# Optimization experiments

Measured on AMD Instinct MI355X. Metric: run time of the kernel, lower is better.

The kernel has to match this reference:

```python
import jax, jax.numpy as jnp
import numpy as np

B, S, D = 1, 2048, 2048
H, KV, HD = 16, 4, 128
HALF = HD // 2
REP = H // KV
LAMBDA_INIT = 0.5
OUT_SCALE = 1.0 - LAMBDA_INIT


def _rope(x, cos, sin):
    # x: (B, S, heads, HD); cos/sin: (S, HD//2). Complex pair rotation on
    # interleaved (even, odd) channels, matching torch.view_as_complex.
    orig_shape = x.shape
    xp = x.reshape(*x.shape[:-1], -1, 2)
    x0, x1 = xp[..., 0], xp[..., 1]
    c = cos[None, :, None, :]
    s = sin[None, :, None, :]
    r0 = x0 * c - x1 * s
    r1 = x0 * s + x1 * c
    return jnp.stack([r0, r1], axis=-1).reshape(orig_shape)


def _sdpa_causal(q, k, v, scale):
    # q,k: (B, S, H, half), v: (B, S, H, HD). Causal softmax attention.
    scores = jnp.einsum('bshd,bthd->bhst', q, k) * scale
    causal = jnp.tril(jnp.ones((S, S), dtype=bool))
    scores = jnp.where(causal[None, None, :, :], scores, jnp.finfo(scores.dtype).min)
    p = jax.nn.softmax(scores, axis=-1)
    return jnp.einsum('bhst,bthd->bshd', p, v)


def setup_inputs() -> dict:
    key = jax.random.key(0)
    ks = jax.random.split(key, 7)
    x = jax.random.normal(ks[0], (B, S, D), dtype=jnp.float32)
    # RoPE frequencies: theta_i = 10000^(-2i/HD), angles = pos * theta
    inv_freq = 1.0 / (10000.0 ** (np.arange(0, HD, 2, dtype=np.float32) / HD))
    angles = np.arange(S, dtype=np.float32)[:, None] * inv_freq[None, :]
    freqs_cos = jnp.asarray(np.cos(angles), dtype=jnp.float32)
    freqs_sin = jnp.asarray(np.sin(angles), dtype=jnp.float32)
    sd = 0.02
    Wq = jax.random.normal(ks[1], (D, H * HD), dtype=jnp.float32) * sd
    Wk = jax.random.normal(ks[2], (D, KV * HD), dtype=jnp.float32) * sd
    Wv = jax.random.normal(ks[3], (D, KV * HD), dtype=jnp.float32) * sd
    Wo = jax.random.normal(ks[4], (H * HD, D), dtype=jnp.float32) * sd
    lam0 = float(np.log(LAMBDA_INIT / (1.0 - LAMBDA_INIT)))
    lambda_param = jnp.full((H,), lam0, dtype=jnp.float32)
    return {'x': x, 'freqs_cos': freqs_cos, 'freqs_sin': freqs_sin,
            'Wq': Wq, 'Wk': Wk, 'Wv': Wv, 'Wo': Wo, 'lambda_param': lambda_param}


def reference(x, freqs_cos, freqs_sin, Wq, Wk, Wv, Wo, lambda_param):
    q = (x @ Wq).reshape(B, S, H, HD)
    k = (x @ Wk).reshape(B, S, KV, HD)
    v = (x @ Wv).reshape(B, S, KV, HD)
    q = _rope(q, freqs_cos, freqs_sin)
    k = _rope(k, freqs_cos, freqs_sin)
    # GQA expansion: each kv head repeated REP times consecutively
    k = jnp.repeat(k, REP, axis=2)
    v = jnp.repeat(v, REP, axis=2)
    q1, q2 = q[..., :HALF], q[..., HALF:]
    k1, k2 = k[..., :HALF], k[..., HALF:]
    scale = 1.0 / jnp.sqrt(jnp.float32(HALF))  # SDPA scales by query last dim
    a1 = _sdpa_causal(q1, k1, v, scale)  # (B, S, H, HD)
    a2 = _sdpa_causal(q2, k2, v, scale)
    lam = jax.nn.sigmoid(lambda_param).astype(x.dtype)[None, None, :, None]
    out = (a1 - lam * a2) * OUT_SCALE
    out = out.reshape(B, S, H * HD)
    return out @ Wo
```

## Files before the change

### kernel.cpp

```cpp
#include <hip/hip_runtime.h>
#include <hip/hip_bf16.h>
#include <cstdint>

typedef __bf16 bf16_t;
typedef __attribute__((ext_vector_type(8))) __bf16 bf16x8;
typedef __attribute__((ext_vector_type(4))) __bf16 bf16x4;
typedef __attribute__((ext_vector_type(4))) float f32x4;

#define S_LEN 2048
#define D_MODEL 2048
#define NH 16
#define NKV 4
#define HD_ 128

#define MFMA16(a, b, c) __builtin_amdgcn_mfma_f32_16x16x32_bf16((a), (b), (c), 0, 0, 0)

__device__ __forceinline__ void gload_lds16(const void* g, void* l) {
  __builtin_amdgcn_global_load_lds((__attribute__((address_space(1))) void*)((void*)g),
                                   (__attribute__((address_space(3))) void*)(l), 16, 0, 0);
}

__global__ __launch_bounds__(256) void cast_x_kernel(const float* __restrict__ in,
                                                     bf16_t* __restrict__ out, int n8) {
  int i = blockIdx.x * 256 + threadIdx.x;
  if (i >= n8) return;
  float4 a = reinterpret_cast<const float4*>(in)[2 * i];
  float4 b = reinterpret_cast<const float4*>(in)[2 * i + 1];
  bf16x8 o = {(__bf16)a.x, (__bf16)a.y, (__bf16)a.z, (__bf16)a.w,
              (__bf16)b.x, (__bf16)b.y, (__bf16)b.z, (__bf16)b.w};
  *reinterpret_cast<bf16x8*>(out + (size_t)i * 8) = o;
}

__global__ __launch_bounds__(256) void transpose_cast64_kernel(const float* __restrict__ in,
    bf16_t* __restrict__ out, int ldin, int ldout) {
  __shared__ float t[64][65];
  const int c0 = blockIdx.x * 64, r0 = blockIdx.y * 64;
  const int rr = threadIdx.x >> 4;
  const int cc = (threadIdx.x & 15) * 4;
#pragma unroll
  for (int p = 0; p < 4; ++p) {
    int r = rr + p * 16;
    float4 v = *reinterpret_cast<const float4*>(in + (size_t)(r0 + r) * ldin + c0 + cc);
    t[r][cc] = v.x; t[r][cc + 1] = v.y; t[r][cc + 2] = v.z; t[r][cc + 3] = v.w;
  }
  __syncthreads();
  const int c = threadIdx.x >> 2;
  const int q = threadIdx.x & 3;
  bf16_t* orow = out + (size_t)(c0 + c) * ldout + r0 + q * 16;
#pragma unroll
  for (int half = 0; half < 2; ++half) {
    bf16x8 o;
#pragma unroll
    for (int j = 0; j < 8; ++j) o[j] = (__bf16)t[q * 16 + half * 8 + j][c];
    *reinterpret_cast<bf16x8*>(orow + half * 8) = o;
  }
}

#define SC_Q 0.18033688f

__global__ __launch_bounds__(256) void rope_kernel(const float* __restrict__ qkv,
    const float* __restrict__ cosT, const float* __restrict__ sinT,
    bf16_t* __restrict__ Qb, bf16_t* __restrict__ Kb) {
  const int s = blockIdx.x;
  const int tid = threadIdx.x;
  const int ch = tid & 15;
  float4 cs = *reinterpret_cast<const float4*>(cosT + s * 64 + ch * 4);
  float4 sn = *reinterpret_cast<const float4*>(sinT + s * 64 + ch * 4);
  {
    const int hq = tid >> 4;
    const float* src = qkv + (size_t)s * 3072 + hq * 128 + ch * 8;
    float4 a = *reinterpret_cast<const float4*>(src);
    float4 b = *reinterpret_cast<const float4*>(src + 4);
    bf16x8 o;
    o[0] = (__bf16)((a.x * cs.x - a.y * sn.x) * SC_Q);
    o[1] = (__bf16)((a.x * sn.x + a.y * cs.x) * SC_Q);
    o[2] = (__bf16)((a.z * cs.y - a.w * sn.y) * SC_Q);
    o[3] = (__bf16)((a.z * sn.y + a.w * cs.y) * SC_Q);
    o[4] = (__bf16)((b.x * cs.z - b.y * sn.z) * SC_Q);
    o[5] = (__bf16)((b.x * sn.z + b.y * cs.z) * SC_Q);
    o[6] = (__bf16)((b.z * cs.w - b.w * sn.w) * SC_Q);
    o[7] = (__bf16)((b.z * sn.w + b.w * cs.w) * SC_Q);
    *reinterpret_cast<bf16x8*>(Qb + ((size_t)hq * S_LEN + s) * HD_ + ch * 8) = o;
  }
  if (tid < 64) {
    const int kh = tid >> 4;
    const float* src = qkv + (size_t)s * 3072 + 2048 + kh * 128 + ch * 8;
    float4 a = *reinterpret_cast<const float4*>(src);
    float4 b = *reinterpret_cast<const float4*>(src + 4);
    bf16x8 o;
    o[0] = (__bf16)(a.x * cs.x - a.y * sn.x);
    o[1] = (__bf16)(a.x * sn.x + a.y * cs.x);
    o[2] = (__bf16)(a.z * cs.y - a.w * sn.y);
    o[3] = (__bf16)(a.z * sn.y + a.w * cs.y);
    o[4] = (__bf16)(b.x * cs.z - b.y * sn.z);
    o[5] = (__bf16)(b.x * sn.z + b.y * cs.z);
    o[6] = (__bf16)(b.z * cs.w - b.w * sn.w);
    o[7] = (__bf16)(b.z * sn.w + b.w * cs.w);
    *reinterpret_cast<bf16x8*>(Kb + ((size_t)kh * S_LEN + s) * HD_ + ch * 8) = o;
  }
}

#define BM 128
#define BK 64

template <int BNv>
__global__ __launch_bounds__(256) void gemm_bf16_kernel(const bf16_t* __restrict__ A,
    const bf16_t* __restrict__ B, float* __restrict__ C, int M, int N, int K) {
  constexpr int NF = BNv / 32;
  constexpr int BITER = BNv * 8 / 256;
  __shared__ __attribute__((aligned(16))) bf16_t aL[BM * BK];
  __shared__ __attribute__((aligned(16))) bf16_t bL[BNv * BK];
  const int tid = threadIdx.x;
  const int wave = tid >> 6, lane = tid & 63;
  const int wr = wave >> 1, wc = wave & 1;
  const int l15 = lane & 15, l4 = lane >> 4;
  const int bm = blockIdx.y * BM, bn = blockIdx.x * BNv;

  f32x4 zero = {0.f, 0.f, 0.f, 0.f};
  f32x4 acc[4][NF];
#pragma unroll
  for (int m = 0; m < 4; ++m)
#pragma unroll
    for (int n = 0; n < NF; ++n) acc[m][n] = zero;

  const bf16_t* aSrc[4];
  bf16_t* aDst[4];
#pragma unroll
  for (int i = 0; i < 4; ++i) {
    int ci = i * 256 + tid;
    int r = ci >> 3;
    int cl = (ci & 7) ^ (r & 7);
    aSrc[i] = A + (size_t)(bm + r) * K + cl * 8;
    aDst[i] = aL + (i * 256 + wave * 64) * 8;
  }
  const bf16_t* bSrc[BITER];
  bf16_t* bDst[BITER];
#pragma unroll
  for (int i = 0; i < BITER; ++i) {
    int ci = i * 256 + tid;
    int r = ci >> 3;
    int cl = (ci & 7) ^ (r & 7);
    bSrc[i] = B + (size_t)(bn + r) * K + cl * 8;
    bDst[i] = bL + (i * 256 + wave * 64) * 8;
  }

  for (int kt = 0; kt < K; kt += BK) {
#pragma unroll
    for (int i = 0; i < 4; ++i) gload_lds16(aSrc[i] + kt, aDst[i]);
#pragma unroll
    for (int i = 0; i < BITER; ++i) gload_lds16(bSrc[i] + kt, bDst[i]);
    __syncthreads();
#pragma unroll
    for (int t = 0; t < 2; ++t) {
      bf16x8 af[4], bfr[NF];
#pragma unroll
      for (int f = 0; f < 4; ++f) {
        int Ra = wr * 64 + f * 16 + l15;
        int ca = (t * 4 + l4) ^ (Ra & 7);
        af[f] = *reinterpret_cast<const bf16x8*>(aL + Ra * 64 + ca * 8);
      }
#pragma unroll
      for (int f = 0; f < NF; ++f) {
        int Rb = wc * (BNv / 2) + f * 16 + l15;
        int cb = (t * 4 + l4) ^ (Rb & 7);
        bfr[f] = *reinterpret_cast<const bf16x8*>(bL + Rb * 64 + cb * 8);
      }
      __builtin_amdgcn_s_setprio(1);
#pragma unroll
      for (int m = 0; m < 4; ++m)
#pragma unroll
        for (int n = 0; n < NF; ++n) acc[m][n] = MFMA16(af[m], bfr[n], acc[m][n]);
      __builtin_amdgcn_s_setprio(0);
    }
    __syncthreads();
  }

#pragma unroll
  for (int m = 0; m < 4; ++m) {
    int row0 = bm + wr * 64 + m * 16 + l4 * 4;
#pragma unroll
    for (int n = 0; n < NF; ++n) {
      int col = bn + wc * (BNv / 2) + n * 16 + l15;
#pragma unroll
      for (int r = 0; r < 4; ++r) C[(size_t)(row0 + r) * N + col] = acc[m][n][r];
    }
  }
}

__global__ __launch_bounds__(256) void diff_attn_kernel(const bf16_t* __restrict__ Qb,
    const bf16_t* __restrict__ Kb, const bf16_t* __restrict__ VTb,
    const float* __restrict__ lambda_param, bf16_t* __restrict__ attn) {
  const int b = blockIdx.x;
  const int p = b >> 1;
  const int h = p >> 4;
  const int tdx = p & 15;
  const int jt = (b & 1) ? tdx : (31 - tdx);
  const int kvh = h >> 2;
  const int tid = threadIdx.x, wave = tid >> 6, lane = tid & 63;
  const int l15 = lane & 15, l4 = lane >> 4;

  __shared__ __attribute__((aligned(16))) bf16_t kB[2][64 * 128];
  __shared__ __attribute__((aligned(16))) bf16_t vB[2][64 * 128];
  __shared__ __attribute__((aligned(16))) bf16_t pS[4][2][16 * 64];

  const bf16_t* kBase = Kb + (size_t)kvh * S_LEN * HD_;
  const bf16_t* vBase = VTb + (size_t)kvh * HD_ * S_LEN;
  int kOff[4], vOff[4], dOff[4];
#pragma unroll
  for (int i = 0; i < 4; ++i) {
    int ci = i * 256 + tid;
    int kr = ci >> 4;
    kOff[i] = kr * HD_ + (((ci & 15) ^ (kr & 7)) * 8);
    int vr = ci >> 3;
    vOff[i] = vr * S_LEN + (((ci & 7) ^ (vr & 7)) * 8);
    dOff[i] = (i * 256 + wave * 64) * 8;
  }

  const float lam = 1.f / (1.f + __expf(-lambda_param[h]));
  const f32x4 zero = {0.f, 0.f, 0.f, 0.f};

  const int q0 = jt * 64;
  const int qg = q0 + wave * 16 + l15;

  const bf16_t* qp = Qb + ((size_t)h * S_LEN + qg) * HD_;
  bf16x8 qf[4];
#pragma unroll
  for (int f = 0; f < 4; ++f) qf[f] = *reinterpret_cast<const bf16x8*>(qp + f * 32 + l4 * 8);

  f32x4 o1[8], o2[8];
#pragma unroll
  for (int n = 0; n < 8; ++n) { o1[n] = zero; o2[n] = zero; }
  float m1 = -__builtin_inff(), m2 = -__builtin_inff(), l1 = 0.f, l2 = 0.f;

#pragma unroll
  for (int i = 0; i < 4; ++i) gload_lds16(kBase + kOff[i], &kB[0][0] + dOff[i]);
#pragma unroll
  for (int i = 0; i < 4; ++i) gload_lds16(vBase + vOff[i], &vB[0][0] + dOff[i]);
  __syncthreads();

  for (int t = 0; t <= jt; ++t) {
    const int cur = t & 1;
    if (t < jt) {
      const size_t kv0n = (size_t)(t + 1) * 64;
#pragma unroll
      for (int i = 0; i < 4; ++i) gload_lds16(kBase + kv0n * HD_ + kOff[i], &kB[cur ^ 1][0] + dOff[i]);
#pragma unroll
      for (int i = 0; i < 4; ++i) gload_lds16(vBase + kv0n + vOff[i], &vB[cur ^ 1][0] + dOff[i]);
    }
    const bf16_t* kL = &kB[cur][0];
    const bf16_t* vL = &vB[cur][0];
    const int kv0 = t * 64;

    f32x4 s1[4], s2[4];
#pragma unroll
    for (int n = 0; n < 4; ++n) { s1[n] = zero; s2[n] = zero; }
    __builtin_amdgcn_s_setprio(1);
#pragma unroll
    for (int tt = 0; tt < 2; ++tt) {
#pragma unroll
      for (int n = 0; n < 4; ++n) {
        const int Rk = n * 16 + l15;
        bf16x8 kf1 = *reinterpret_cast<const bf16x8*>(kL + Rk * 128 + (((tt * 4 + l4) ^ (Rk & 7)) * 8));
        s1[n] = MFMA16(kf1, qf[tt], s1[n]);
      }
    }
#pragma unroll
    for (int tt = 0; tt < 2; ++tt) {
#pragma unroll
      for (int n = 0; n < 4; ++n) {
        const int Rk = n * 16 + l15;
        bf16x8 kf2 = *reinterpret_cast<const bf16x8*>(kL + Rk * 128 + (((8 + tt * 4 + l4) ^ (Rk & 7)) * 8));
        s2[n] = MFMA16(kf2, qf[2 + tt], s2[n]);
      }
    }
    __builtin_amdgcn_s_setprio(0);

    if (t == jt) {
#pragma unroll
      for (int n = 0; n < 4; ++n)
#pragma unroll
        for (int r = 0; r < 4; ++r)
          if (kv0 + n * 16 + l4 * 4 + r > qg) { s1[n][r] = -1e30f; s2[n][r] = -1e30f; }
    }

    {
      float ma[4];
#pragma unroll
      for (int n = 0; n < 4; ++n)
        ma[n] = fmaxf(fmaxf(s1[n][0], s1[n][1]), fmaxf(s1[n][2], s1[n][3]));
      float tmax = fmaxf(fmaxf(ma[0], ma[1]), fmaxf(ma[2], ma[3]));
      tmax = fmaxf(tmax, __shfl_xor(tmax, 16));
      tmax = fmaxf(tmax, __shfl_xor(tmax, 32));
      if (!__all(tmax <= m1 + 8.f)) {
        const float mn = fmaxf(m1, tmax);
        const float sc = __builtin_exp2f(m1 - mn);
        m1 = mn;
        l1 *= sc;
#pragma unroll
        for (int n = 0; n < 8; ++n) o1[n] *= sc;
      }
      float rsn[4];
#pragma unroll
      for (int n = 0; n < 4; ++n) {
        float e0 = __builtin_exp2f(s1[n][0] - m1);
        float e1 = __builtin_exp2f(s1[n][1] - m1);
        float e2 = __builtin_exp2f(s1[n][2] - m1);
        float e3 = __builtin_exp2f(s1[n][3] - m1);
        rsn[n] = (e0 + e1) + (e2 + e3);
        int cswz = (n * 2 + (l4 >> 1)) ^ (l15 & 7);
        bf16x4 pk = {(__bf16)e0, (__bf16)e1, (__bf16)e2, (__bf16)e3};
        *reinterpret_cast<bf16x4*>(&pS[wave][0][l15 * 64 + cswz * 8 + (l4 & 1) * 4]) = pk;
      }
      float rs = (rsn[0] + rsn[1]) + (rsn[2] + rsn[3]);
      rs += __shfl_xor(rs, 16);
      rs += __shfl_xor(rs, 32);
      l1 += rs;
    }
    {
      float ma[4];
#pragma unroll
      for (int n = 0; n < 4; ++n)
        ma[n] = fmaxf(fmaxf(s2[n][0], s2[n][1]), fmaxf(s2[n][2], s2[n][3]));
      float tmax = fmaxf(fmaxf(ma[0], ma[1]), fmaxf(ma[2], ma[3]));
      tmax = fmaxf(tmax, __shfl_xor(tmax, 16));
      tmax = fmaxf(tmax, __shfl_xor(tmax, 32));
      if (!__all(tmax <= m2 + 8.f)) {
        const float mn = fmaxf(m2, tmax);
        const float sc = __builtin_exp2f(m2 - mn);
        m2 = mn;
        l2 *= sc;
#pragma unroll
        for (int n = 0; n < 8; ++n) o2[n] *= sc;
      }
      float rsn[4];
#pragma unroll
      for (int n = 0; n < 4; ++n) {
        float e0 = __builtin_exp2f(s2[n][0] - m2);
        float e1 = __builtin_exp2f(s2[n][1] - m2);
        float e2 = __builtin_exp2f(s2[n][2] - m2);
        float e3 = __builtin_exp2f(s2[n][3] - m2);
        rsn[n] = (e0 + e1) + (e2 + e3);
        int cswz = (n * 2 + (l4 >> 1)) ^ (l15 & 7);
        bf16x4 pk = {(__bf16)e0, (__bf16)e1, (__bf16)e2, (__bf16)e3};
        *reinterpret_cast<bf16x4*>(&pS[wave][1][l15 * 64 + cswz * 8 + (l4 & 1) * 4]) = pk;
      }
      float rs = (rsn[0] + rsn[1]) + (rsn[2] + rsn[3]);
      rs += __shfl_xor(rs, 16);
      rs += __shfl_xor(rs, 32);
      l2 += rs;
    }

    __builtin_amdgcn_s_setprio(1);
#pragma unroll
    for (int kt = 0; kt < 2; ++kt) {
      int cp = ((kt * 4 + l4) ^ (l15 & 7)) * 8;
      bf16x8 pf1 = *reinterpret_cast<const bf16x8*>(&pS[wave][0][l15 * 64 + cp]);
      bf16x8 pf2 = *reinterpret_cast<const bf16x8*>(&pS[wave][1][l15 * 64 + cp]);
#pragma unroll
      for (int n = 0; n < 8; ++n) {
        const int Rv = n * 16 + l15;
        bf16x8 vf = *reinterpret_cast<const bf16x8*>(vL + Rv * 64 + (((kt * 4 + l4) ^ (Rv & 7)) * 8));
        o1[n] = MFMA16(vf, pf1, o1[n]);
        o2[n] = MFMA16(vf, pf2, o2[n]);
      }
    }
    __builtin_amdgcn_s_setprio(0);
    __syncthreads();
  }

  const float i1 = 1.f / l1, i2 = lam / l2;
  bf16_t* orow = attn + (size_t)qg * D_MODEL + h * HD_;
#pragma unroll
  for (int n = 0; n < 8; ++n) {
    bf16x4 w = {(__bf16)((o1[n][0] * i1 - o2[n][0] * i2) * 0.5f),
                (__bf16)((o1[n][1] * i1 - o2[n][1] * i2) * 0.5f),
                (__bf16)((o1[n][2] * i1 - o2[n][2] * i2) * 0.5f),
                (__bf16)((o1[n][3] * i1 - o2[n][3] * i2) * 0.5f)};
    *reinterpret_cast<bf16x4*>(orow + n * 16 + l4 * 4) = w;
  }
}

extern "C" void kernel_launch(void* const* d_in, const int* in_sizes, int n_in,
                              void* d_out, int out_size, void* d_ws, size_t ws_size,
                              hipStream_t stream) {
  const float* x    = (const float*)d_in[0];
  const float* fcos = (const float*)d_in[1];
  const float* fsin = (const float*)d_in[2];
  const float* Wq   = (const float*)d_in[3];
  const float* Wk   = (const float*)d_in[4];
  const float* Wv   = (const float*)d_in[5];
  const float* Wo   = (const float*)d_in[6];
  const float* lam  = (const float*)d_in[7];
  float* out = (float*)d_out;

  char* w = (char*)d_ws;
  bf16_t* xb    = (bf16_t*)(w);
  bf16_t* attnb = (bf16_t*)(w);
  bf16_t* WqkvT = (bf16_t*)(w + (8ull << 20));
  bf16_t* Qb    = (bf16_t*)(w + (8ull << 20));
  bf16_t* Kb    = (bf16_t*)(w + (16ull << 20));
  bf16_t* VT    = (bf16_t*)(w + (18ull << 20));
  bf16_t* WoT   = (bf16_t*)(w + (20ull << 20));
  float*  QKV   = (float*) (w + (28ull << 20));

  cast_x_kernel<<<2048, 256, 0, stream>>>(x, xb, 524288);
  transpose_cast64_kernel<<<dim3(32, 32), 256, 0, stream>>>(Wq, WqkvT, 2048, 2048);
  transpose_cast64_kernel<<<dim3(8, 32), 256, 0, stream>>>(Wk, WqkvT + 2048 * 2048, 512, 2048);
  transpose_cast64_kernel<<<dim3(8, 32), 256, 0, stream>>>(Wv, WqkvT + 2560 * 2048, 512, 2048);
  transpose_cast64_kernel<<<dim3(32, 32), 256, 0, stream>>>(Wo, WoT, 2048, 2048);

  gemm_bf16_kernel<64><<<dim3(48, 16), 256, 0, stream>>>(xb, WqkvT, QKV, 2048, 3072, 2048);

  rope_kernel<<<2048, 256, 0, stream>>>(QKV, fcos, fsin, Qb, Kb);
  transpose_cast64_kernel<<<dim3(8, 32), 256, 0, stream>>>(QKV + 2560, VT, 3072, 2048);

  diff_attn_kernel<<<512, 256, 0, stream>>>(Qb, Kb, VT, lam, attnb);

  gemm_bf16_kernel<64><<<dim3(32, 16), 256, 0, stream>>>(attnb, WoT, out, 2048, 2048, 2048);
}
```

Measured before the change: 286.5 us.

## Pair long and short causal query tiles per block and serialize the two softmax branches

After: 278.7 us. 1.03x faster.

```diff
diff --git a/kernel.cpp b/kernel.cpp
--- a/kernel.cpp
+++ b/kernel.cpp
@@ -190,18 +190,15 @@
 __global__ __launch_bounds__(256) void diff_attn_kernel(const bf16_t* __restrict__ Qb,
     const bf16_t* __restrict__ Kb, const bf16_t* __restrict__ VTb,
     const float* __restrict__ lambda_param, bf16_t* __restrict__ attn) {
-  const int b = blockIdx.x;
-  const int p = b >> 1;
-  const int h = p >> 4;
-  const int tdx = p & 15;
-  const int jt = (b & 1) ? tdx : (31 - tdx);
+  const int h = blockIdx.x >> 4;
+  const int pr = blockIdx.x & 15;
   const int kvh = h >> 2;
   const int tid = threadIdx.x, wave = tid >> 6, lane = tid & 63;
   const int l15 = lane & 15, l4 = lane >> 4;
 
   __shared__ __attribute__((aligned(16))) bf16_t kB[2][64 * 128];
   __shared__ __attribute__((aligned(16))) bf16_t vB[2][64 * 128];
-  __shared__ __attribute__((aligned(16))) bf16_t pS[4][2][16 * 64];
+  __shared__ __attribute__((aligned(16))) bf16_t pS[4][16 * 64];
 
   const bf16_t* kBase = Kb + (size_t)kvh * S_LEN * HD_;
   const bf16_t* vBase = VTb + (size_t)kvh * HD_ * S_LEN;
@@ -219,164 +216,189 @@
   const float lam = 1.f / (1.f + __expf(-lambda_param[h]));
   const f32x4 zero = {0.f, 0.f, 0.f, 0.f};
 
-  const int q0 = jt * 64;
-  const int qg = q0 + wave * 16 + l15;
-
-  const bf16_t* qp = Qb + ((size_t)h * S_LEN + qg) * HD_;
-  bf16x8 qf[4];
-#pragma unroll
-  for (int f = 0; f < 4; ++f) qf[f] = *reinterpret_cast<const bf16x8*>(qp + f * 32 + l4 * 8);
-
-  f32x4 o1[8], o2[8];
-#pragma unroll
-  for (int n = 0; n < 8; ++n) { o1[n] = zero; o2[n] = zero; }
-  float m1 = -__builtin_inff(), m2 = -__builtin_inff(), l1 = 0.f, l2 = 0.f;
-
-#pragma unroll
-  for (int i = 0; i < 4; ++i) gload_lds16(kBase + kOff[i], &kB[0][0] + dOff[i]);
-#pragma unroll
-  for (int i = 0; i < 4; ++i) gload_lds16(vBase + vOff[i], &vB[0][0] + dOff[i]);
-  __syncthreads();
-
-  for (int t = 0; t <= jt; ++t) {
-    const int cur = t & 1;
-    if (t < jt) {
-      const size_t kv0n = (size_t)(t + 1) * 64;
-#pragma unroll
-      for (int i = 0; i < 4; ++i) gload_lds16(kBase + kv0n * HD_ + kOff[i], &kB[cur ^ 1][0] + dOff[i]);
-#pragma unroll
-      for (int i = 0; i < 4; ++i) gload_lds16(vBase + kv0n + vOff[i], &vB[cur ^ 1][0] + dOff[i]);
+  for (int ph = 0; ph < 2; ++ph) {
+    const int jt = (ph == 0) ? (31 - pr) : pr;
+    const int q0 = jt * 64;
+    const int qg = q0 + wave * 16 + l15;
+
+    const bf16_t* qp = Qb + ((size_t)h * S_LEN + qg) * HD_;
+    bf16x8 qf[4];
+#pragma unroll
+    for (int f = 0; f < 4; ++f) qf[f] = *reinterpret_cast<const bf16x8*>(qp + f * 32 + l4 * 8);
+
+    f32x4 o1[8], o2[8];
+#pragma unroll
+    for (int n = 0; n < 8; ++n) { o1[n] = zero; o2[n] = zero; }
+    float m1 = -__builtin_inff(), m2 = -__builtin_inff(), l1 = 0.f, l2 = 0.f;
+
+#pragma unroll
+    for (int i = 0; i < 4; ++i) gload_lds16(kBase + kOff[i], &kB[0][0] + dOff[i]);
+#pragma unroll
+    for (int i = 0; i < 4; ++i) gload_lds16(vBase + vOff[i], &vB[0][0] + dOff[i]);
+    __syncthreads();
+
+    for (int t = 0; t <= jt; ++t) {
+      const int cur = t & 1;
+      if (t < jt) {
+        const size_t kv0n = (size_t)(t + 1) * 64;
+#pragma unroll
+        for (int i = 0; i < 4; ++i) gload_lds16(kBase + kv0n * HD_ + kOff[i], &kB[cur ^ 1][0] + dOff[i]);
+#pragma unroll
+        for (int i = 0; i < 4; ++i) gload_lds16(vBase + kv0n + vOff[i], &vB[cur ^ 1][0] + dOff[i]);
+      }
+      const bf16_t* kL = &kB[cur][0];
+      const bf16_t* vL = &vB[cur][0];
+      const int kv0 = t * 64;
+      const bool diag = (t == jt);
+
+      f32x4 s1[4];
+#pragma unroll
+      for (int n = 0; n < 4; ++n) s1[n] = zero;
+      __builtin_amdgcn_s_setprio(1);
+#pragma unroll
+      for (int tt = 0; tt < 2; ++tt) {
+#pragma unroll
+        for (int n = 0; n < 4; ++n) {
+          const int Rk = n * 16 + l15;
+          bf16x8 kf = *reinterpret_cast<const bf16x8*>(kL + Rk * 128 + (((tt * 4 + l4) ^ (Rk & 7)) * 8));
+          s1[n] = MFMA16(kf, qf[tt], s1[n]);
+        }
+      }
+      __builtin_amdgcn_s_setprio(0);
+      if (diag) {
+#pragma unroll
+        for (int n = 0; n < 4; ++n)
+#pragma unroll
+          for (int r = 0; r < 4; ++r)
+            if (kv0 + n * 16 + l4 * 4 + r > qg) s1[n][r] = -1e30f;
+      }
+      {
+        float ma[4];
+#pragma unroll
+        for (int n = 0; n < 4; ++n)
+          ma[n] = fmaxf(fmaxf(s1[n][0], s1[n][1]), fmaxf(s1[n][2], s1[n][3]));
+        float tmax = fmaxf(fmaxf(ma[0], ma[1]), fmaxf(ma[2], ma[3]));
+        tmax = fmaxf(tmax, __shfl_xor(tmax, 16));
+        tmax = fmaxf(tmax, __shfl_xor(tmax, 32));
+        if (!__all(tmax <= m1 + 8.f)) {
+          const float mn = fmaxf(m1, tmax);
+          const float sc = __builtin_exp2f(m1 - mn);
+          m1 = mn;
+          l1 *= sc;
+#pragma unroll
+          for (int n = 0; n < 8; ++n) o1[n] *= sc;
+        }
+        float rsn[4];
+#pragma unroll
+        for (int n = 0; n < 4; ++n) {
+          float e0 = __builtin_exp2f(s1[n][0] - m1);
+          float e1 = __builtin_exp2f(s1[n][1] - m1);
+          float e2 = __builtin_exp2f(s1[n][2] - m1);
+          float e3 = __builtin_exp2f(s1[n][3] - m1);
+          rsn[n] = (e0 + e1) + (e2 + e3);
+          int cswz = (n * 2 + (l4 >> 1)) ^ (l15 & 7);
+          bf16x4 pk = {(__bf16)e0, (__bf16)e1, (__bf16)e2, (__bf16)e3};
+          *reinterpret_cast<bf16x4*>(&pS[wave][l15 * 64 + cswz * 8 + (l4 & 1) * 4]) = pk;
+        }
+        float rs = (rsn[0] + rsn[1]) + (rsn[2] + rsn[3]);
+        rs += __shfl_xor(rs, 16);
+        rs += __shfl_xor(rs, 32);
+        l1 += rs;
+      }
+      __builtin_amdgcn_s_setprio(1);
+#pragma unroll
+      for (int kt = 0; kt < 2; ++kt) {
+        int cp = ((kt * 4 + l4) ^ (l15 & 7)) * 8;
+        bf16x8 pf = *reinterpret_cast<const bf16x8*>(&pS[wave][l15 * 64 + cp]);
+#pragma unroll
+        for (int n = 0; n < 8; ++n) {
+          const int Rv = n * 16 + l15;
+          bf16x8 vf = *reinterpret_cast<const bf16x8*>(vL + Rv * 64 + (((kt * 4 + l4) ^ (Rv & 7)) * 8));
+          o1[n] = MFMA16(vf, pf, o1[n]);
+        }
+      }
+      __builtin_amdgcn_s_setprio(0);
+
+      f32x4 s2[4];
+#pragma unroll
+      for (int n = 0; n < 4; ++n) s2[n] = zero;
+      __builtin_amdgcn_s_setprio(1);
+#pragma unroll
+      for (int tt = 0; tt < 2; ++tt) {
+#pragma unroll
+        for (int n = 0; n < 4; ++n) {
+          const int Rk = n * 16 + l15;
+          bf16x8 kf = *reinterpret_cast<const bf16x8*>(kL + Rk * 128 + (((8 + tt * 4 + l4) ^ (Rk & 7)) * 8));
+          s2[n] = MFMA16(kf, qf[2 + tt], s2[n]);
+        }
+      }
+      __builtin_amdgcn_s_setprio(0);
+      if (diag) {
+#pragma unroll
+        for (int n = 0; n < 4; ++n)
+#pragma unroll
+          for (int r = 0; r < 4; ++r)
+            if (kv0 + n * 16 + l4 * 4 + r > qg) s2[n][r] = -1e30f;
+      }
+      {
+        float ma[4];
+#pragma unroll
+        for (int n = 0; n < 4; ++n)
+          ma[n] = fmaxf(fmaxf(s2[n][0], s2[n][1]), fmaxf(s2[n][2], s2[n][3]));
+        float tmax = fmaxf(fmaxf(ma[0], ma[1]), fmaxf(ma[2], ma[3]));
+        tmax = fmaxf(tmax, __shfl_xor(tmax, 16));
+        tmax = fmaxf(tmax, __shfl_xor(tmax, 32));
+        if (!__all(tmax <= m2 + 8.f)) {
+          const float mn = fmaxf(m2, tmax);
+          const float sc = __builtin_exp2f(m2 - mn);
+          m2 = mn;
+          l2 *= sc;
+#pragma unroll
+          for (int n = 0; n < 8; ++n) o2[n] *= sc;
+        }
+        float rsn[4];
+#pragma unroll
+        for (int n = 0; n < 4; ++n) {
+          float e0 = __builtin_exp2f(s2[n][0] - m2);
+          float e1 = __builtin_exp2f(s2[n][1] - m2);
+          float e2 = __builtin_exp2f(s2[n][2] - m2);
+          float e3 = __builtin_exp2f(s2[n][3] - m2);
+          rsn[n] = (e0 + e1) + (e2 + e3);
+          int cswz = (n * 2 + (l4 >> 1)) ^ (l15 & 7);
+          bf16x4 pk = {(__bf16)e0, (__bf16)e1, (__bf16)e2, (__bf16)e3};
+          *reinterpret_cast<bf16x4*>(&pS[wave][l15 * 64 + cswz * 8 + (l4 & 1) * 4]) = pk;
+        }
+        float rs = (rsn[0] + rsn[1]) + (rsn[2] + rsn[3]);
+        rs += __shfl_xor(rs, 16);
+        rs += __shfl_xor(rs, 32);
+        l2 += rs;
+      }
+      __builtin_amdgcn_s_setprio(1);
+#pragma unroll
+      for (int kt = 0; kt < 2; ++kt) {
+        int cp = ((kt * 4 + l4) ^ (l15 & 7)) * 8;
+        bf16x8 pf = *reinterpret_cast<const bf16x8*>(&pS[wave][l15 * 64 + cp]);
+#pragma unroll
+        for (int n = 0; n < 8; ++n) {
+          const int Rv = n * 16 + l15;
+          bf16x8 vf = *reinterpret_cast<const bf16x8*>(vL + Rv * 64 + (((kt * 4 + l4) ^ (Rv & 7)) * 8));
+          o2[n] = MFMA16(vf, pf, o2[n]);
+        }
+      }
+      __builtin_amdgcn_s_setprio(0);
+      __syncthreads();
     }
-    const bf16_t* kL = &kB[cur][0];
-    const bf16_t* vL = &vB[cur][0];
-    const int kv0 = t * 64;
-
-    f32x4 s1[4], s2[4];
-#pragma unroll
-    for (int n = 0; n < 4; ++n) { s1[n] = zero; s2[n] = zero; }
-    __builtin_amdgcn_s_setprio(1);
-#pragma unroll
-    for (int tt = 0; tt < 2; ++tt) {
-#pragma unroll
-      for (int n = 0; n < 4; ++n) {
-        const int Rk = n * 16 + l15;
-        bf16x8 kf1 = *reinterpret_cast<const bf16x8*>(kL + Rk * 128 + (((tt * 4 + l4) ^ (Rk & 7)) * 8));
-        s1[n] = MFMA16(kf1, qf[tt], s1[n]);
-      }
+
+    const float i1 = 1.f / l1, i2 = lam / l2;
+    bf16_t* orow = attn + (size_t)qg * D_MODEL + h * HD_;
+#pragma unroll
+    for (int n = 0; n < 8; ++n) {
+      bf16x4 w = {(__bf16)((o1[n][0] * i1 - o2[n][0] * i2) * 0.5f),
+                  (__bf16)((o1[n][1] * i1 - o2[n][1] * i2) * 0.5f),
+                  (__bf16)((o1[n][2] * i1 - o2[n][2] * i2) * 0.5f),
+                  (__bf16)((o1[n][3] * i1 - o2[n][3] * i2) * 0.5f)};
+      *reinterpret_cast<bf16x4*>(orow + n * 16 + l4 * 4) = w;
     }
-#pragma unroll
-    for (int tt = 0; tt < 2; ++tt) {
-#pragma unroll
-      for (int n = 0; n < 4; ++n) {
-        const int Rk = n * 16 + l15;
-        bf16x8 kf2 = *reinterpret_cast<const bf16x8*>(kL + Rk * 128 + (((8 + tt * 4 + l4) ^ (Rk & 7)) * 8));
-        s2[n] = MFMA16(kf2, qf[2 + tt], s2[n]);
-      }
-    }
-    __builtin_amdgcn_s_setprio(0);
-
-    if (t == jt) {
-#pragma unroll
-      for (int n = 0; n < 4; ++n)
-#pragma unroll
-        for (int r = 0; r < 4; ++r)
-          if (kv0 + n * 16 + l4 * 4 + r > qg) { s1[n][r] = -1e30f; s2[n][r] = -1e30f; }
-    }
-
-    {
-      float ma[4];
-#pragma unroll
-      for (int n = 0; n < 4; ++n)
-        ma[n] = fmaxf(fmaxf(s1[n][0], s1[n][1]), fmaxf(s1[n][2], s1[n][3]));
-      float tmax = fmaxf(fmaxf(ma[0], ma[1]), fmaxf(ma[2], ma[3]));
-      tmax = fmaxf(tmax, __shfl_xor(tmax, 16));
-      tmax = fmaxf(tmax, __shfl_xor(tmax, 32));
-      if (!__all(tmax <= m1 + 8.f)) {
-        const float mn = fmaxf(m1, tmax);
-        const float sc = __builtin_exp2f(m1 - mn);
-        m1 = mn;
-        l1 *= sc;
-#pragma unroll
-        for (int n = 0; n < 8; ++n) o1[n] *= sc;
-      }
-      float rsn[4];
-#pragma unroll
-      for (int n = 0; n < 4; ++n) {
-        float e0 = __builtin_exp2f(s1[n][0] - m1);
-        float e1 = __builtin_exp2f(s1[n][1] - m1);
-        float e2 = __builtin_exp2f(s1[n][2] - m1);
-        float e3 = __builtin_exp2f(s1[n][3] - m1);
-        rsn[n] = (e0 + e1) + (e2 + e3);
-        int cswz = (n * 2 + (l4 >> 1)) ^ (l15 & 7);
-        bf16x4 pk = {(__bf16)e0, (__bf16)e1, (__bf16)e2, (__bf16)e3};
-        *reinterpret_cast<bf16x4*>(&pS[wave][0][l15 * 64 + cswz * 8 + (l4 & 1) * 4]) = pk;
-      }
-      float rs = (rsn[0] + rsn[1]) + (rsn[2] + rsn[3]);
-      rs += __shfl_xor(rs, 16);
-      rs += __shfl_xor(rs, 32);
-      l1 += rs;
-    }
-    {
-      float ma[4];
-#pragma unroll
-      for (int n = 0; n < 4; ++n)
-        ma[n] = fmaxf(fmaxf(s2[n][0], s2[n][1]), fmaxf(s2[n][2], s2[n][3]));
-      float tmax = fmaxf(fmaxf(ma[0], ma[1]), fmaxf(ma[2], ma[3]));
-      tmax = fmaxf(tmax, __shfl_xor(tmax, 16));
-      tmax = fmaxf(tmax, __shfl_xor(tmax, 32));
-      if (!__all(tmax <= m2 + 8.f)) {
-        const float mn = fmaxf(m2, tmax);
-        const float sc = __builtin_exp2f(m2 - mn);
-        m2 = mn;
-        l2 *= sc;
-#pragma unroll
-        for (int n = 0; n < 8; ++n) o2[n] *= sc;
-      }
-      float rsn[4];
-#pragma unroll
-      for (int n = 0; n < 4; ++n) {
-        float e0 = __builtin_exp2f(s2[n][0] - m2);
-        float e1 = __builtin_exp2f(s2[n][1] - m2);
-        float e2 = __builtin_exp2f(s2[n][2] - m2);
-        float e3 = __builtin_exp2f(s2[n][3] - m2);
-        rsn[n] = (e0 + e1) + (e2 + e3);
-        int cswz = (n * 2 + (l4 >> 1)) ^ (l15 & 7);
-        bf16x4 pk = {(__bf16)e0, (__bf16)e1, (__bf16)e2, (__bf16)e3};
-        *reinterpret_cast<bf16x4*>(&pS[wave][1][l15 * 64 + cswz * 8 + (l4 & 1) * 4]) = pk;
-      }
-      float rs = (rsn[0] + rsn[1]) + (rsn[2] + rsn[3]);
-      rs += __shfl_xor(rs, 16);
-      rs += __shfl_xor(rs, 32);
-      l2 += rs;
-    }
-
-    __builtin_amdgcn_s_setprio(1);
-#pragma unroll
-    for (int kt = 0; kt < 2; ++kt) {
-      int cp = ((kt * 4 + l4) ^ (l15 & 7)) * 8;
-      bf16x8 pf1 = *reinterpret_cast<const bf16x8*>(&pS[wave][0][l15 * 64 + cp]);
-      bf16x8 pf2 = *reinterpret_cast<const bf16x8*>(&pS[wave][1][l15 * 64 + cp]);
-#pragma unroll
-      for (int n = 0; n < 8; ++n) {
-        const int Rv = n * 16 + l15;
-        bf16x8 vf = *reinterpret_cast<const bf16x8*>(vL + Rv * 64 + (((kt * 4 + l4) ^ (Rv & 7)) * 8));
-        o1[n] = MFMA16(vf, pf1, o1[n]);
-        o2[n] = MFMA16(vf, pf2, o2[n]);
-      }
-    }
-    __builtin_amdgcn_s_setprio(0);
-    __syncthreads();
-  }
-
-  const float i1 = 1.f / l1, i2 = lam / l2;
-  bf16_t* orow = attn + (size_t)qg * D_MODEL + h * HD_;
-#pragma unroll
-  for (int n = 0; n < 8; ++n) {
-    bf16x4 w = {(__bf16)((o1[n][0] * i1 - o2[n][0] * i2) * 0.5f),
-                (__bf16)((o1[n][1] * i1 - o2[n][1] * i2) * 0.5f),
-                (__bf16)((o1[n][2] * i1 - o2[n][2] * i2) * 0.5f),
-                (__bf16)((o1[n][3] * i1 - o2[n][3] * i2) * 0.5f)};
-    *reinterpret_cast<bf16x4*>(orow + n * 16 + l4 * 4) = w;
   }
 }
 
@@ -414,7 +436,7 @@
   rope_kernel<<<2048, 256, 0, stream>>>(QKV, fcos, fsin, Qb, Kb);
   transpose_cast64_kernel<<<dim3(8, 32), 256, 0, stream>>>(QKV + 2560, VT, 3072, 2048);
 
-  diff_attn_kernel<<<512, 256, 0, stream>>>(Qb, Kb, VT, lam, attnb);
+  diff_attn_kernel<<<256, 256, 0, stream>>>(Qb, Kb, VT, lam, attnb);
 
   gemm_bf16_kernel<64><<<dim3(32, 16), 256, 0, stream>>>(attnb, WoT, out, 2048, 2048, 2048);
 }
```
